# Performance work log

Measured on AMD Instinct MI355X. Metric: run time of the kernel, lower is better.

## Reference

```python
import jax, jax.numpy as jnp
import numpy as np

V_TH = 1.0  # IF neuron threshold (default v_threshold=1, v_reset=0)
SCALE = 1.0  # PoissonEncoder firing scale


def setup_inputs() -> dict:
    key = jax.random.key(0)
    k_x, k_n, k_w1, k_w2 = jax.random.split(key, 4)
    B, T, D_IN, D_H, D_OUT = 8192, 32, 784, 100, 10
    x = jax.random.uniform(k_x, (B, D_IN), dtype=jnp.float32)
    noise = jax.random.uniform(k_n, (T, B, D_IN), dtype=jnp.float32)
    W1 = jax.random.normal(k_w1, (D_H, D_IN), dtype=jnp.float32) * (1.0 / np.sqrt(D_IN))
    W2 = jax.random.normal(k_w2, (D_OUT, D_H), dtype=jnp.float32) * (1.0 / np.sqrt(D_H))
    return {"x": x, "noise": noise, "W1": W1, "W2": W2}


def reference(x, noise, W1, W2):
    # Poisson encoding: spike if uniform noise < scale * firing_rate.  [T,B,784]
    spikes = jnp.where(noise < SCALE * x[None, :, :], 1.0, 0.0).astype(x.dtype)

    B = x.shape[0]
    v0 = jnp.zeros((B, W1.shape[0]), dtype=x.dtype)          # membrane potential [B,100]
    logits0 = jnp.zeros((B, W2.shape[0]), dtype=x.dtype)      # accumulated logits [B,10]

    def step(carry, sp_t):
        v, logits = carry
        h = jnp.einsum('bi,hi->bh', sp_t, W1)                 # Linear 784->100 (no bias)
        v = v + h                                             # integrate
        spike = jnp.where(v - V_TH > 0, 1.0, 0.0).astype(h.dtype)  # fire
        v = v - spike * V_TH                                  # soft reset
        logits = logits + jnp.einsum('bh,oh->bo', spike, W2)  # Linear 100->10, accumulate
        return (v, logits), None

    (_, logits), _ = jax.lax.scan(step, (v0, logits0), spikes)
    return logits
```

## Files before the change

kernel.cpp:

```cpp
#include <hip/hip_runtime.h>
#include <hip/hip_bf16.h>
#include <cstdint>


typedef __attribute__((ext_vector_type(8))) short bf16x8;
typedef __attribute__((ext_vector_type(4))) float f32x4;

#define D_IN 784
#define NB 8192
#define KT 25
#define NTL 8
#define DH 100

__global__ void prep_w1(const float* __restrict__ W1, unsigned short* __restrict__ wf) {
    int idx = blockIdx.x * 256 + threadIdx.x;
    if (idx >= KT * NTL * 64) return;
    int l  = idx & 63;
    int nt = (idx >> 6) & 7;
    int kt = idx >> 9;
    int n  = nt * 16 + (l & 15);
    int i0 = kt * 32 + (l >> 4) * 8;
    size_t fbase = (size_t)(kt * 8 + nt) * 1024;
    #pragma unroll
    for (int j = 0; j < 8; ++j) {
        int i = i0 + j;
        float w = (n < DH && i < D_IN) ? W1[n * D_IN + i] : 0.f;
        uint32_t ub = __float_as_uint(w);
        uint32_t rh = ub + 0x7FFFu + ((ub >> 16) & 1u);
        unsigned short h = (unsigned short)(rh >> 16);
        float hf = __uint_as_float(((uint32_t)h) << 16);
        float resid = w - hf;
        uint32_t ul = __float_as_uint(resid);
        uint32_t rl = ul + 0x7FFFu + ((ul >> 16) & 1u);
        unsigned short lo = (unsigned short)(rl >> 16);
        wf[fbase + l * 8 + j]       = h;
        wf[fbase + 512 + l * 8 + j] = lo;
    }
}

__global__ __launch_bounds__(256) void snn_fused(const float* __restrict__ x,
                                                 const float* __restrict__ noise,
                                                 const unsigned short* __restrict__ wf,
                                                 float* __restrict__ H) {
    __shared__ __align__(4) unsigned short sB[128 * 50];
    const int tid  = threadIdx.x;
    const int lane = tid & 63;
    const int wave = tid >> 6;
    const int L     = blockIdx.x;
    const int btile = (L & 7) * 8 + ((L >> 3) & 7);
    const int t     = L >> 6;
    const int b0    = btile * 128;
    const float* nb = noise + (size_t)t * ((size_t)NB * D_IN) + (size_t)b0 * D_IN;
    const float* xb = x + (size_t)b0 * D_IN;

    if (tid < 128) sB[tid * 50 + 49] = 0;

    {
        const int u = lane & 15;
        float4 nA, xA;
        nA = *reinterpret_cast<const float4*>(nb + (size_t)tid * 4);
        xA = *reinterpret_cast<const float4*>(xb + (size_t)tid * 4);
        #pragma unroll 2
        for (int p = 0; p < 98; ++p) {
            const float4 nC = nA, xC = xA;
            if (p < 97) {
                const size_t fo = (size_t)(p + 1) * 256 + tid;
                nA = *reinterpret_cast<const float4*>(nb + fo * 4);
                xA = *reinterpret_cast<const float4*>(xb + fo * 4);
            }
            const unsigned long long m0 = __ballot(nC.x < xC.x);
            const unsigned long long m1 = __ballot(nC.y < xC.y);
            const unsigned long long m2 = __ballot(nC.z < xC.z);
            const unsigned long long m3 = __ballot(nC.w < xC.w);
            if (lane < 16) {
                const uint32_t v = (uint32_t)((m0 >> (4 * u)) & 15ull)
                                 | ((uint32_t)((m1 >> (4 * u)) & 15ull) << 4)
                                 | ((uint32_t)((m2 >> (4 * u)) & 15ull) << 8)
                                 | ((uint32_t)((m3 >> (4 * u)) & 15ull) << 12);
                const int g = p * 64 + wave * 16 + u;
                const uint32_t row = ((uint32_t)g * 42800u) >> 21;
                const int colu = g - (int)row * 49;
                sB[row * 50 + colu] = (unsigned short)v;
            }
        }
    }
    __syncthreads();

    const int Mhalf = wave >> 1;
    const int Nhalf = wave & 1;
    const int rowLoc = Mhalf * 64 + (lane & 15);
    const int lg     = lane >> 4;
    const int qe0    = (lg & 1) * 2 + (lg >> 1) * 16;
    const uint32_t* s32 = reinterpret_cast<const uint32_t*>(sB);

    f32x4 acc[4][4];
    #pragma unroll
    for (int i = 0; i < 4; ++i)
        #pragma unroll
        for (int j = 0; j < 4; ++j) acc[i][j] = (f32x4){0.f, 0.f, 0.f, 0.f};

    #pragma unroll 2
    for (int kt = 0; kt < KT; ++kt) {
        uint32_t g[4];
        #pragma unroll
        for (int mt = 0; mt < 4; ++mt) g[mt] = s32[(rowLoc + mt * 16) * 25 + kt];

        bf16x8 afr[4];
        #pragma unroll
        for (int mt = 0; mt < 4; ++mt) {
            union { uint32_t u[4]; bf16x8 v; } pk;
            #pragma unroll
            for (int d = 0; d < 4; ++d) {
                const int qe = qe0 + (d & 1) * 8 + (d >> 1);
                pk.u[d] = ((g[mt] >> qe) & 1u) * 0x3F80u
                        | ((g[mt] >> (qe + 4)) & 1u) * 0x3F800000u;
            }
            afr[mt] = pk.v;
        }
        #pragma unroll
        for (int nt = 0; nt < 4; ++nt) {
            const size_t fo = (size_t)(kt * 8 + Nhalf * 4 + nt) * 1024 + lane * 8;
            const bf16x8 bhi = *reinterpret_cast<const bf16x8*>(wf + fo);
            const bf16x8 blo = *reinterpret_cast<const bf16x8*>(wf + fo + 512);
            #pragma unroll
            for (int mt = 0; mt < 4; ++mt) {
                acc[mt][nt] = __builtin_amdgcn_mfma_f32_16x16x32_bf16(afr[mt], bhi, acc[mt][nt], 0, 0, 0);
                acc[mt][nt] = __builtin_amdgcn_mfma_f32_16x16x32_bf16(afr[mt], blo, acc[mt][nt], 0, 0, 0);
            }
        }
    }
    const int colBase   = Nhalf * 64 + (lane & 15);
    const int rowInTile = (lane >> 4) * 4;
    #pragma unroll
    for (int mt = 0; mt < 4; ++mt) {
        const int rowG = b0 + Mhalf * 64 + mt * 16 + rowInTile;
        #pragma unroll
        for (int nt = 0; nt < 4; ++nt) {
            const int col = colBase + nt * 16;
            if (col < DH) {
                #pragma unroll
                for (int r = 0; r < 4; ++r)
                    H[(size_t)(rowG + r) * (32 * DH) + t * DH + col] = acc[mt][nt][r];
            }
        }
    }
}

__global__ __launch_bounds__(256) void snn_scan(const float* __restrict__ H,
                                                const float* __restrict__ W2,
                                                float* __restrict__ out) {
    __shared__ float cbuf[2][104];
    __shared__ float w2s[1000];
    const int tid = threadIdx.x;
    const int r = tid >> 7, h = tid & 127;
    const size_t b = (size_t)blockIdx.x * 2 + r;
    for (int i = tid; i < 1000; i += 256) w2s[i] = W2[i];

    float cnt = 0.f;
    if (h < DH) {
        float hv[32];
        #pragma unroll
        for (int t = 0; t < 32; ++t) hv[t] = H[b * (32 * DH) + t * DH + h];
        float v = 0.f;
        #pragma unroll
        for (int t = 0; t < 32; ++t) {
            v += hv[t];
            float s = (v - 1.0f > 0.0f) ? 1.0f : 0.0f;
            v -= s;
            cnt += s;
        }
    }
    if (h < DH) cbuf[r][h] = cnt;
    __syncthreads();
    if (tid < 20) {
        const int rr = tid / 10, o = tid % 10;
        float s = 0.f;
        for (int hh = 0; hh < DH; ++hh) s += cbuf[rr][hh] * w2s[o * DH + hh];
        out[((size_t)blockIdx.x * 2 + rr) * 10 + o] = s;
    }
}

extern "C" void kernel_launch(void* const* d_in, const int* in_sizes, int n_in,
                              void* d_out, int out_size, void* d_ws, size_t ws_size,
                              hipStream_t stream) {
    const float* x     = (const float*)d_in[0];
    const float* noise = (const float*)d_in[1];
    const float* W1    = (const float*)d_in[2];
    const float* W2    = (const float*)d_in[3];
    float* out = (float*)d_out;

    unsigned short* wf = (unsigned short*)d_ws;
    float* H = (float*)((char*)d_ws + (1u << 20));

    prep_w1<<<50, 256, 0, stream>>>(W1, wf);
    snn_fused<<<2048, 256, 0, stream>>>(x, noise, wf, H);
    snn_scan<<<4096, 256, 0, stream>>>(H, W2, out);
}
```

Baseline: 328.7 us.

## Process two timesteps per block to reuse x loads and W1 fragments

```diff
diff --git a/kernel.cpp b/kernel.cpp
--- a/kernel.cpp
+++ b/kernel.cpp
@@ -9,12 +9,11 @@
 #define D_IN 784
 #define NB 8192
 #define KT 25
-#define NTL 8
 #define DH 100
 
 __global__ void prep_w1(const float* __restrict__ W1, unsigned short* __restrict__ wf) {
     int idx = blockIdx.x * 256 + threadIdx.x;
-    if (idx >= KT * NTL * 64) return;
+    if (idx >= KT * 8 * 64) return;
     int l  = idx & 63;
     int nt = (idx >> 6) & 7;
     int kt = idx >> 9;
@@ -38,109 +37,138 @@
     }
 }
 
-__global__ __launch_bounds__(256) void snn_fused(const float* __restrict__ x,
+__device__ __forceinline__ f32x4 ldnt(const float* p) {
+    return __builtin_nontemporal_load(reinterpret_cast<const f32x4*>(p));
+}
+__device__ __forceinline__ f32x4 ld(const float* p) {
+    return *reinterpret_cast<const f32x4*>(p);
+}
+
+__global__ __launch_bounds__(512) void snn_gemm2(const float* __restrict__ x,
                                                  const float* __restrict__ noise,
                                                  const unsigned short* __restrict__ wf,
                                                  float* __restrict__ H) {
-    __shared__ __align__(4) unsigned short sB[128 * 50];
+    __shared__ __align__(4) unsigned short sB[2][128 * 50];
     const int tid  = threadIdx.x;
     const int lane = tid & 63;
     const int wave = tid >> 6;
     const int L     = blockIdx.x;
     const int btile = (L & 7) * 8 + ((L >> 3) & 7);
-    const int t     = L >> 6;
+    const int tp    = L >> 6;
     const int b0    = btile * 128;
-    const float* nb = noise + (size_t)t * ((size_t)NB * D_IN) + (size_t)b0 * D_IN;
-    const float* xb = x + (size_t)b0 * D_IN;
-
-    if (tid < 128) sB[tid * 50 + 49] = 0;
+    const int u     = lane & 15;
+    const int lg    = lane >> 4;
+    const int Mhalf = wave >> 2;
+    const int Nq    = wave & 3;
+
+    if (tid < 256) sB[tid >> 7][(tid & 127) * 50 + 49] = 0;
+
+    const float* xb    = x + (size_t)b0 * D_IN;
+    const float* nb0   = noise + (size_t)(2 * tp) * ((size_t)NB * D_IN) + (size_t)b0 * D_IN;
+    const float* nb1   = nb0 + (size_t)NB * D_IN;
 
     {
-        const int u = lane & 15;
-        float4 nA, xA;
-        nA = *reinterpret_cast<const float4*>(nb + (size_t)tid * 4);
-        xA = *reinterpret_cast<const float4*>(xb + (size_t)tid * 4);
+        f32x4 xA, n0A, n1A;
+        {
+            const size_t fo = (size_t)tid * 4;
+            xA  = ld(xb + fo);
+            n0A = ldnt(nb0 + fo);
+            n1A = ldnt(nb1 + fo);
+        }
         #pragma unroll 2
-        for (int p = 0; p < 98; ++p) {
-            const float4 nC = nA, xC = xA;
-            if (p < 97) {
-                const size_t fo = (size_t)(p + 1) * 256 + tid;
-                nA = *reinterpret_cast<const float4*>(nb + fo * 4);
-                xA = *reinterpret_cast<const float4*>(xb + fo * 4);
-            }
-            const unsigned long long m0 = __ballot(nC.x < xC.x);
-            const unsigned long long m1 = __ballot(nC.y < xC.y);
-            const unsigned long long m2 = __ballot(nC.z < xC.z);
-            const unsigned long long m3 = __ballot(nC.w < xC.w);
+        for (int p = 0; p < 49; ++p) {
+            const f32x4 xC = xA, n0C = n0A, n1C = n1A;
+            if (p < 48) {
+                const size_t fo = (size_t)(p + 1) * 2048 + (size_t)tid * 4;
+                xA  = ld(xb + fo);
+                n0A = ldnt(nb0 + fo);
+                n1A = ldnt(nb1 + fo);
+            }
+            const unsigned long long a0 = __ballot(n0C[0] < xC[0]);
+            const unsigned long long a1 = __ballot(n0C[1] < xC[1]);
+            const unsigned long long a2 = __ballot(n0C[2] < xC[2]);
+            const unsigned long long a3 = __ballot(n0C[3] < xC[3]);
+            const unsigned long long c0 = __ballot(n1C[0] < xC[0]);
+            const unsigned long long c1 = __ballot(n1C[1] < xC[1]);
+            const unsigned long long c2 = __ballot(n1C[2] < xC[2]);
+            const unsigned long long c3 = __ballot(n1C[3] < xC[3]);
             if (lane < 16) {
-                const uint32_t v = (uint32_t)((m0 >> (4 * u)) & 15ull)
-                                 | ((uint32_t)((m1 >> (4 * u)) & 15ull) << 4)
-                                 | ((uint32_t)((m2 >> (4 * u)) & 15ull) << 8)
-                                 | ((uint32_t)((m3 >> (4 * u)) & 15ull) << 12);
-                const int g = p * 64 + wave * 16 + u;
+                const int g = p * 128 + wave * 16 + u;
                 const uint32_t row = ((uint32_t)g * 42800u) >> 21;
-                const int colu = g - (int)row * 49;
-                sB[row * 50 + colu] = (unsigned short)v;
+                const int off = (int)row * 50 + (g - (int)row * 49);
+                const uint32_t v0 = (uint32_t)((a0 >> (4 * u)) & 15ull)
+                                  | ((uint32_t)((a1 >> (4 * u)) & 15ull) << 4)
+                                  | ((uint32_t)((a2 >> (4 * u)) & 15ull) << 8)
+                                  | ((uint32_t)((a3 >> (4 * u)) & 15ull) << 12);
+                const uint32_t v1 = (uint32_t)((c0 >> (4 * u)) & 15ull)
+                                  | ((uint32_t)((c1 >> (4 * u)) & 15ull) << 4)
+                                  | ((uint32_t)((c2 >> (4 * u)) & 15ull) << 8)
+                                  | ((uint32_t)((c3 >> (4 * u)) & 15ull) << 12);
+                sB[0][off] = (unsigned short)v0;
+                sB[1][off] = (unsigned short)v1;
             }
         }
     }
     __syncthreads();
 
-    const int Mhalf = wave >> 1;
-    const int Nhalf = wave & 1;
-    const int rowLoc = Mhalf * 64 + (lane & 15);
-    const int lg     = lane >> 4;
-    const int qe0    = (lg & 1) * 2 + (lg >> 1) * 16;
-    const uint32_t* s32 = reinterpret_cast<const uint32_t*>(sB);
-
-    f32x4 acc[4][4];
+    const uint32_t* s0 = reinterpret_cast<const uint32_t*>(&sB[0][0]);
+    const uint32_t* s1 = reinterpret_cast<const uint32_t*>(&sB[1][0]);
+    const int qe0 = (lg & 1) * 2 + (lg >> 1) * 16;
+    const int rowBase = (Mhalf * 64 + u) * 25;
+
+    f32x4 acc[2][4][2];
     #pragma unroll
-    for (int i = 0; i < 4; ++i)
-        #pragma unroll
-        for (int j = 0; j < 4; ++j) acc[i][j] = (f32x4){0.f, 0.f, 0.f, 0.f};
+    for (int tt = 0; tt < 2; ++tt)
+        #pragma unroll
+        for (int mt = 0; mt < 4; ++mt)
+            #pragma unroll
+            for (int nt = 0; nt < 2; ++nt) acc[tt][mt][nt] = (f32x4){0, 0, 0, 0};
 
     #pragma unroll 2
     for (int kt = 0; kt < KT; ++kt) {
-        uint32_t g[4];
-        #pragma unroll
-        for (int mt = 0; mt < 4; ++mt) g[mt] = s32[(rowLoc + mt * 16) * 25 + kt];
-
-        bf16x8 afr[4];
+        bf16x8 bhi[2], blo[2];
+        #pragma unroll
+        for (int nt = 0; nt < 2; ++nt) {
+            const size_t fo = (size_t)(kt * 8 + Nq * 2 + nt) * 1024 + lane * 8;
+            bhi[nt] = *reinterpret_cast<const bf16x8*>(wf + fo);
+            blo[nt] = *reinterpret_cast<const bf16x8*>(wf + fo + 512);
+        }
         #pragma unroll
         for (int mt = 0; mt < 4; ++mt) {
-            union { uint32_t u[4]; bf16x8 v; } pk;
+            const int ro = rowBase + mt * 400 + kt;
+            const uint32_t g0 = s0[ro];
+            const uint32_t g1 = s1[ro];
+            union { uint32_t uu[4]; bf16x8 vv; } pk0, pk1;
             #pragma unroll
             for (int d = 0; d < 4; ++d) {
                 const int qe = qe0 + (d & 1) * 8 + (d >> 1);
-                pk.u[d] = ((g[mt] >> qe) & 1u) * 0x3F80u
-                        | ((g[mt] >> (qe + 4)) & 1u) * 0x3F800000u;
-            }
-            afr[mt] = pk.v;
-        }
-        #pragma unroll
-        for (int nt = 0; nt < 4; ++nt) {
-            const size_t fo = (size_t)(kt * 8 + Nhalf * 4 + nt) * 1024 + lane * 8;
-            const bf16x8 bhi = *reinterpret_cast<const bf16x8*>(wf + fo);
-            const bf16x8 blo = *reinterpret_cast<const bf16x8*>(wf + fo + 512);
-            #pragma unroll
-            for (int mt = 0; mt < 4; ++mt) {
-                acc[mt][nt] = __builtin_amdgcn_mfma_f32_16x16x32_bf16(afr[mt], bhi, acc[mt][nt], 0, 0, 0);
-                acc[mt][nt] = __builtin_amdgcn_mfma_f32_16x16x32_bf16(afr[mt], blo, acc[mt][nt], 0, 0, 0);
-            }
-        }
-    }
-    const int colBase   = Nhalf * 64 + (lane & 15);
-    const int rowInTile = (lane >> 4) * 4;
+                pk0.uu[d] = ((g0 >> qe) & 1u) * 0x3F80u | ((g0 >> (qe + 4)) & 1u) * 0x3F800000u;
+                pk1.uu[d] = ((g1 >> qe) & 1u) * 0x3F80u | ((g1 >> (qe + 4)) & 1u) * 0x3F800000u;
+            }
+            #pragma unroll
+            for (int nt = 0; nt < 2; ++nt) {
+                acc[0][mt][nt] = __builtin_amdgcn_mfma_f32_16x16x32_bf16(pk0.vv, bhi[nt], acc[0][mt][nt], 0, 0, 0);
+                acc[0][mt][nt] = __builtin_amdgcn_mfma_f32_16x16x32_bf16(pk0.vv, blo[nt], acc[0][mt][nt], 0, 0, 0);
+                acc[1][mt][nt] = __builtin_amdgcn_mfma_f32_16x16x32_bf16(pk1.vv, bhi[nt], acc[1][mt][nt], 0, 0, 0);
+                acc[1][mt][nt] = __builtin_amdgcn_mfma_f32_16x16x32_bf16(pk1.vv, blo[nt], acc[1][mt][nt], 0, 0, 0);
+            }
+        }
+    }
+
     #pragma unroll
-    for (int mt = 0; mt < 4; ++mt) {
-        const int rowG = b0 + Mhalf * 64 + mt * 16 + rowInTile;
-        #pragma unroll
-        for (int nt = 0; nt < 4; ++nt) {
-            const int col = colBase + nt * 16;
-            if (col < DH) {
-                #pragma unroll
-                for (int r = 0; r < 4; ++r)
-                    H[(size_t)(rowG + r) * (32 * DH) + t * DH + col] = acc[mt][nt][r];
+    for (int tt = 0; tt < 2; ++tt) {
+        const int t = 2 * tp + tt;
+        #pragma unroll
+        for (int mt = 0; mt < 4; ++mt) {
+            const int rowG = b0 + Mhalf * 64 + mt * 16 + lg * 4;
+            #pragma unroll
+            for (int nt = 0; nt < 2; ++nt) {
+                const int col = (Nq * 2 + nt) * 16 + u;
+                if (col < DH) {
+                    #pragma unroll
+                    for (int r = 0; r < 4; ++r)
+                        H[(size_t)(rowG + r) * (32 * DH) + t * DH + col] = acc[tt][mt][nt][r];
+                }
             }
         }
     }
@@ -193,6 +221,6 @@
     float* H = (float*)((char*)d_ws + (1u << 20));
 
     prep_w1<<<50, 256, 0, stream>>>(W1, wf);
-    snn_fused<<<2048, 256, 0, stream>>>(x, noise, wf, H);
+    snn_gemm2<<<1024, 512, 0, stream>>>(x, noise, wf, H);
     snn_scan<<<4096, 256, 0, stream>>>(H, W2, out);
 }
```

After: 317.5 us, median of 2. 1.04x faster.
